# Performance work log

Measured on AMD Instinct MI355X. Metric: run time of the kernel, lower is better.

## Reference

```python
import jax, jax.numpy as jnp
import numpy as np

INPUT_SIZE = 512
HIDDEN = 768
NUM_ARMS = 32
LAMBD = 1.0
NU = 0.1


def setup_inputs() -> dict:
    key = jax.random.key(0)
    ks = jax.random.split(key, 10)
    H, I, A = HIDDEN, INPUT_SIZE, NUM_ARMS
    inp = {
        "x": jax.random.normal(ks[0], (I,), dtype=jnp.float32),
        "previous_reward": jax.random.normal(ks[1], (1, 1), dtype=jnp.float32),
        "h0": jnp.zeros((1, 1, H), dtype=jnp.float32),
        "c0": jnp.zeros((1, 1, H), dtype=jnp.float32),
        # LSTM params, torch layout: W_ih [4H, I+1], W_hh [4H, H], biases [4H]
        "W_ih": jax.random.normal(ks[2], (4 * H, I + 1), dtype=jnp.float32) * 0.05,
        "W_hh": jax.random.normal(ks[3], (4 * H, H), dtype=jnp.float32) * 0.05,
        "b_ih": jax.random.normal(ks[4], (4 * H,), dtype=jnp.float32) * 0.05,
        "b_hh": jax.random.normal(ks[5], (4 * H,), dtype=jnp.float32) * 0.05,
        "fc_W": jax.random.normal(ks[6], (A, H), dtype=jnp.float32) * 0.05,
        "fc_b": jax.random.normal(ks[7], (A,), dtype=jnp.float32) * 0.05,
    }
    total_param = (4 * H * (I + 1)) + (4 * H * H) + (4 * H) + (4 * H) + (A * H) + A
    inp["U"] = LAMBD * jnp.ones((total_param,), dtype=jnp.float32)
    return inp


def _lstm_arm_rewards(params, xin, h, c):
    """Single-step LSTM (torch gate order i,f,g,o) + reward head."""
    W_ih, W_hh, b_ih, b_hh, fc_W, fc_b = params
    gates = W_ih @ xin + b_ih + W_hh @ h + b_hh  # [4H]
    i, f, g, o = jnp.split(gates, 4)
    i, f, o = jax.nn.sigmoid(i), jax.nn.sigmoid(f), jax.nn.sigmoid(o)
    g = jnp.tanh(g)
    c_new = f * c + i * g
    h_new = o * jnp.tanh(c_new)
    rewards = fc_W @ h_new + fc_b  # [A]
    return rewards, (h_new, c_new)


def reference(x, previous_reward, h0, c0, W_ih, W_hh, b_ih, b_hh, fc_W, fc_b, U):
    A = fc_b.shape[0]
    xin = jnp.concatenate([x, previous_reward.reshape(-1)])  # [I+1]
    h, c = h0.reshape(-1), c0.reshape(-1)
    params = (W_ih, W_hh, b_ih, b_hh, fc_W, fc_b)

    rewards, (h_new, c_new) = _lstm_arm_rewards(params, xin, h, c)
    arm_probs = jax.nn.softmax(rewards)

    # Per-arm gradients d rewards[i] / d params, flattened in torch param order.
    jac = jax.jacrev(lambda p: _lstm_arm_rewards(p, xin, h, c)[0])(params)
    G_lstm = jnp.concatenate([jac[k].reshape(A, -1) for k in range(4)], axis=1)
    # fc_rewards grads are never zeroed in the original (only lstm.zero_grad()),
    # so they accumulate over the arm loop -> cumulative sum over arms.
    G_fc = jnp.cumsum(
        jnp.concatenate([jac[4].reshape(A, -1), jac[5].reshape(A, -1)], axis=1), axis=0
    )
    G = jnp.concatenate([G_lstm, G_fc], axis=1)  # [A, total_param]

    sigma = jnp.sqrt(jnp.sum(LAMBD * G * G / U, axis=1))  # [A]
    ucb = NU * sigma

    selected_arm = jnp.argmax(rewards + ucb)
    selected_reward = rewards[selected_arm].reshape(1, 1)
    U_new = U + G[selected_arm] ** 2

    return (
        selected_reward,
        arm_probs.reshape(1, -1),
        selected_arm,
        h_new.reshape(1, 1, -1),
        c_new.reshape(1, 1, -1),
        U_new,
    )
```

## Files before the change

kernel.cpp:

```cpp
#include <hip/hip_runtime.h>
#include <math.h>

#define H 768
#define ISZ 512
#define IN1 513
#define NARM 32
#define NU_C 0.1f

#define U_WIH 0
#define U_WHH (3072*513)
#define U_BIH (U_WHH + 3072*768)
#define U_BHH (U_BIH + 3072)
#define U_FCW (U_BHH + 3072)
#define U_FCB (U_FCW + 32*768)

#define O_SELR 0
#define O_PROB 1
#define O_SELA 33
#define O_HN   34
#define O_CN   (34+768)
#define O_U    (34+768+768)

#define W_D    0
#define W_T    3072
#define W_HN   6144
#define W_SEL  6912
#define W_HZ   6913

__device__ inline float wave_reduce(float v) {
    for (int d = 32; d > 0; d >>= 1) v += __shfl_xor(v, d, 64);
    return v;
}

__device__ inline float frcp(float x) { return __builtin_amdgcn_rcpf(x); }

__device__ inline void store_f4_as_2xf2(float* p, float4 v) {
    *(float2*)p = make_float2(v.x, v.y);
    *(float2*)(p + 2) = make_float2(v.z, v.w);
}

__global__ __launch_bounds__(256) void k_prep(
    const float* __restrict__ x, const float* __restrict__ prevr,
    const float* __restrict__ h0, const float* __restrict__ c0,
    const float* __restrict__ Wih, const float* __restrict__ Whh,
    const float* __restrict__ bih, const float* __restrict__ bhh,
    const float* __restrict__ U,
    float* __restrict__ out, float* __restrict__ ws)
{
    int wave = threadIdx.x >> 6;
    int lane = threadIdx.x & 63;
    const float pr = prevr[0];

    float4 hv4[3];
    bool nzb = false;
    #pragma unroll
    for (int it = 0; it < 3; ++it) {
        hv4[it] = *(const float4*)(h0 + (lane + it * 64) * 4);
        nzb |= (hv4[it].x != 0.f) || (hv4[it].y != 0.f) ||
               (hv4[it].z != 0.f) || (hv4[it].w != 0.f);
    }
    const bool hnz = (__ballot(nzb) != 0ull);

    if (blockIdx.x < 192) {
        int j = blockIdx.x * 4 + wave;
        float a0 = 0.f, a1 = 0.f, a2 = 0.f, a3 = 0.f;
        const float* r0 = Wih + (size_t)(0*H + j) * IN1;
        const float* r1 = Wih + (size_t)(1*H + j) * IN1;
        const float* r2 = Wih + (size_t)(2*H + j) * IN1;
        const float* r3 = Wih + (size_t)(3*H + j) * IN1;
        for (int k = lane; k < IN1; k += 64) {
            float xv = (k < ISZ) ? x[k] : pr;
            a0 += r0[k] * xv; a1 += r1[k] * xv; a2 += r2[k] * xv; a3 += r3[k] * xv;
        }
        if (hnz) {
            const float* s0 = Whh + (size_t)(0*H + j) * H;
            const float* s1 = Whh + (size_t)(1*H + j) * H;
            const float* s2 = Whh + (size_t)(2*H + j) * H;
            const float* s3 = Whh + (size_t)(3*H + j) * H;
            #pragma unroll
            for (int it = 0; it < 3; ++it) {
                int c = (lane + it * 64) * 4;
                float4 h4 = hv4[it];
                float4 w;
                w = *(const float4*)(s0 + c);
                a0 += w.x*h4.x + w.y*h4.y + w.z*h4.z + w.w*h4.w;
                w = *(const float4*)(s1 + c);
                a1 += w.x*h4.x + w.y*h4.y + w.z*h4.z + w.w*h4.w;
                w = *(const float4*)(s2 + c);
                a2 += w.x*h4.x + w.y*h4.y + w.z*h4.z + w.w*h4.w;
                w = *(const float4*)(s3 + c);
                a3 += w.x*h4.x + w.y*h4.y + w.z*h4.z + w.w*h4.w;
            }
        }
        a0 = wave_reduce(a0); a1 = wave_reduce(a1);
        a2 = wave_reduce(a2); a3 = wave_reduce(a3);
        if (lane == 0) {
            float zi = a0 + bih[0*H + j] + bhh[0*H + j];
            float zf = a1 + bih[1*H + j] + bhh[1*H + j];
            float zg = a2 + bih[2*H + j] + bhh[2*H + j];
            float zo = a3 + bih[3*H + j] + bhh[3*H + j];
            float ig = 1.f / (1.f + expf(-zi));
            float fg = 1.f / (1.f + expf(-zf));
            float gg = tanhf(zg);
            float og = 1.f / (1.f + expf(-zo));
            float cj = c0[j];
            float cn = fg * cj + ig * gg;
            float t  = tanhf(cn);
            float hn = og * t;
            float dtc = og * (1.f - t * t);
            ws[W_D + 0*H + j] = dtc * gg * ig * (1.f - ig);
            ws[W_D + 1*H + j] = dtc * cj * fg * (1.f - fg);
            ws[W_D + 2*H + j] = dtc * ig * (1.f - gg * gg);
            ws[W_D + 3*H + j] = t * og * (1.f - og);
            ws[W_HN + j] = hn;
            out[O_HN + j] = hn;
            out[O_CN + j] = cn;
        }
    } else {
        int r = (blockIdx.x - 192) * 4 + wave;
        const float* uih = U + U_WIH + (size_t)r * IN1;
        float acc = 0.f;
        for (int k = lane; k < IN1; k += 64) {
            float xv = (k < ISZ) ? x[k] : pr;
            acc += xv * xv * frcp(uih[k]);
        }
        if (hnz) {
            const float* uhh = U + U_WHH + (size_t)r * H;
            #pragma unroll
            for (int it = 0; it < 3; ++it) {
                int c = (lane + it * 64) * 4;
                float4 u4 = *(const float4*)(uhh + c);
                float4 h4 = hv4[it];
                acc += h4.x*h4.x*frcp(u4.x) + h4.y*h4.y*frcp(u4.y)
                     + h4.z*h4.z*frcp(u4.z) + h4.w*h4.w*frcp(u4.w);
            }
        }
        acc = wave_reduce(acc);
        if (lane == 0)
            ws[W_T + r] = acc + frcp(U[U_BIH + r]) + frcp(U[U_BHH + r]);
    }
}

__global__ __launch_bounds__(1024) void k_armsfinal(
    const float* __restrict__ fcW, const float* __restrict__ fcb,
    const float* __restrict__ h0, const float* __restrict__ U,
    float* __restrict__ out, float* __restrict__ ws)
{
    __shared__ float wsum_s[H];
    __shared__ float hn_s[H];
    __shared__ float r_s[NARM], s_s[NARM], q_s[NARM];
    __shared__ int nzflag;
    int t = threadIdx.x;
    if (t == 0) nzflag = 0;
    __syncthreads();
    if (t < H) {
        float d0 = ws[W_D + 0*H + t], T0 = ws[W_T + 0*H + t];
        float d1 = ws[W_D + 1*H + t], T1 = ws[W_T + 1*H + t];
        float d2 = ws[W_D + 2*H + t], T2 = ws[W_T + 2*H + t];
        float d3 = ws[W_D + 3*H + t], T3 = ws[W_T + 3*H + t];
        wsum_s[t] = d0*d0*T0 + d1*d1*T1 + d2*d2*T2 + d3*d3*T3;
        hn_s[t] = ws[W_HN + t];
        if (h0[t] != 0.f) atomicOr(&nzflag, 1);
    }
    __syncthreads();
    int wave = t >> 6, lane = t & 63;
    for (int a = wave; a < NARM; a += 16) {
        const float* frow = fcW + (size_t)a * H;
        const float* urow = U + U_FCW + (size_t)a * H;
        float ar = 0.f, as = 0.f, aq = 0.f;
        #pragma unroll
        for (int it = 0; it < 3; ++it) {
            int j = lane * 4 + it * 256;
            float4 f4 = *(const float4*)(frow + j);
            float4 u4 = *(const float4*)(urow + j);
            float4 h4 = *(const float4*)(&hn_s[j]);
            float4 w4 = *(const float4*)(&wsum_s[j]);
            ar += f4.x*h4.x + f4.y*h4.y + f4.z*h4.z + f4.w*h4.w;
            as += f4.x*f4.x*w4.x + f4.y*f4.y*w4.y + f4.z*f4.z*w4.z + f4.w*f4.w*w4.w;
            aq += h4.x*h4.x*frcp(u4.x) + h4.y*h4.y*frcp(u4.y)
                + h4.z*h4.z*frcp(u4.z) + h4.w*h4.w*frcp(u4.w);
        }
        ar = wave_reduce(ar); as = wave_reduce(as); aq = wave_reduce(aq);
        if (lane == 0) {
            r_s[a] = ar + fcb[a];
            s_s[a] = as;
            q_s[a] = aq + frcp(U[U_FCB + a]);
        }
    }
    __syncthreads();
    if (t == 0) ((int*)ws)[W_HZ] = nzflag;
    if (t < NARM) {
        float r = r_s[t];
        float s = s_s[t];
        float q = q_s[t];
        float cum = q;
        for (int d = 1; d < 32; d <<= 1) {
            float v = __shfl_up(cum, d, 32);
            if (t >= d) cum += v;
        }
        float sc = r + NU_C * sqrtf(s + cum);
        float best = sc; int sel = t;
        for (int d = 16; d > 0; d >>= 1) {
            float ob = __shfl_xor(best, d, 32);
            int   oi = __shfl_xor(sel, d, 32);
            if (ob > best || (ob == best && oi < sel)) { best = ob; sel = oi; }
        }
        float mx = r;
        for (int d = 16; d > 0; d >>= 1) mx = fmaxf(mx, __shfl_xor(mx, d, 32));
        float e = expf(r - mx);
        float se = e;
        for (int d = 16; d > 0; d >>= 1) se += __shfl_xor(se, d, 32);
        out[O_PROB + t] = e / se;
        float rsel = __shfl(r, sel, 32);
        if (t == 0) {
            out[O_SELR] = rsel;
            out[O_SELA] = (float)sel;
            ((int*)ws)[W_SEL] = sel;
        }
    }
}

#define B_A 3072
#define B_B (B_A + 2304)
#define B_C (B_B + 6)
#define B_D (B_C + 24)
__global__ __launch_bounds__(256) void k_unew(
    const float* __restrict__ x, const float* __restrict__ prevr,
    const float* __restrict__ h0, const float* __restrict__ fcW,
    const float* __restrict__ U, float* __restrict__ out,
    const float* __restrict__ ws)
{
    const int sel = ((const int*)ws)[W_SEL];
    const int hnz = ((const int*)ws)[W_HZ];
    int b = blockIdx.x, t = threadIdx.x;
    float* Un = out + O_U;
    if (b < B_A) {
        int g = b / H, j = b - g * H;
        float s = fcW[(size_t)sel * H + j] * ws[W_D + g*H + j];
        float s2 = s * s;
        const float* u = U + U_WIH + (size_t)b * IN1;
        float* o = Un + U_WIH + (size_t)b * IN1;
        float xv1 = x[t];
        float xv2 = x[t + 256];
        o[t]       = u[t]       + s2 * xv1 * xv1;
        o[t + 256] = u[t + 256] + s2 * xv2 * xv2;
        if (t == 0) {
            float pr = prevr[0];
            o[512] = u[512] + s2 * pr * pr;
        }
    } else if (b < B_B) {
        int i4 = (b - B_A) * 256 + t;
        int e = i4 * 4;
        float4 u4 = *(const float4*)(U + U_WHH + e);
        float4 o4;
        if (hnz) {
            int r = e / H;
            int g = r / H, j = r - g * H;
            int k = e - r * H;
            float s = fcW[(size_t)sel * H + j] * ws[W_D + g*H + j];
            float s2 = s * s;
            float4 h4 = *(const float4*)(h0 + k);
            o4.x = u4.x + s2 * h4.x * h4.x;
            o4.y = u4.y + s2 * h4.y * h4.y;
            o4.z = u4.z + s2 * h4.z * h4.z;
            o4.w = u4.w + s2 * h4.w * h4.w;
        } else {
            o4 = u4;
        }
        store_f4_as_2xf2(Un + U_WHH + e, o4);
    } else if (b < B_C) {
        int m = ((b - B_B) * 256 + t) * 4;
        int r = (m < 3072) ? m : m - 3072;
        int g = r / H, j = r - g * H;
        float4 f4 = *(const float4*)(fcW + (size_t)sel * H + j);
        float4 d4 = *(const float4*)(ws + W_D + g*H + j);
        float4 u4 = *(const float4*)(U + U_BIH + m);
        float4 o4;
        float sx = f4.x*d4.x, sy = f4.y*d4.y, sz = f4.z*d4.z, sw = f4.w*d4.w;
        o4.x = u4.x + sx*sx; o4.y = u4.y + sy*sy;
        o4.z = u4.z + sz*sz; o4.w = u4.w + sw*sw;
        store_f4_as_2xf2(Un + U_BIH + m, o4);
    } else if (b < B_D) {
        int e = ((b - B_C) * 256 + t) * 4;
        int a = e / H, j = e - a * H;
        float4 h4 = *(const float4*)(ws + W_HN + j);
        float4 u4 = *(const float4*)(U + U_FCW + e);
        float m = (a <= sel) ? 1.f : 0.f;
        float4 o4;
        o4.x = u4.x + m * h4.x * h4.x;
        o4.y = u4.y + m * h4.y * h4.y;
        o4.z = u4.z + m * h4.z * h4.z;
        o4.w = u4.w + m * h4.w * h4.w;
        store_f4_as_2xf2(Un + U_FCW + e, o4);
    } else {
        if (t < NARM)
            Un[U_FCB + t] = U[U_FCB + t] + ((t <= sel) ? 1.f : 0.f);
    }
}

extern "C" void kernel_launch(void* const* d_in, const int* in_sizes, int n_in,
                              void* d_out, int out_size, void* d_ws, size_t ws_size,
                              hipStream_t stream) {
    const float* x     = (const float*)d_in[0];
    const float* prevr = (const float*)d_in[1];
    const float* h0    = (const float*)d_in[2];
    const float* c0    = (const float*)d_in[3];
    const float* Wih   = (const float*)d_in[4];
    const float* Whh   = (const float*)d_in[5];
    const float* bih   = (const float*)d_in[6];
    const float* bhh   = (const float*)d_in[7];
    const float* fcW   = (const float*)d_in[8];
    const float* fcb   = (const float*)d_in[9];
    const float* U     = (const float*)d_in[10];
    float* out = (float*)d_out;
    float* ws  = (float*)d_ws;

    hipLaunchKernelGGL(k_prep, dim3(960), dim3(256), 0, stream,
                       x, prevr, h0, c0, Wih, Whh, bih, bhh, U, out, ws);
    hipLaunchKernelGGL(k_armsfinal, dim3(1), dim3(1024), 0, stream,
                       fcW, fcb, h0, U, out, ws);
    hipLaunchKernelGGL(k_unew, dim3(B_D + 1), dim3(256), 0, stream,
                       x, prevr, h0, fcW, U, out, ws);
}
```

Before: 23.38 us.

## Fuse gate, U-weighted norm and arm partials into prep; move W_hh U copy earlier

After: 28.60 us. +22.3%, slower.

```diff
diff --git a/kernel.cpp b/kernel.cpp
--- a/kernel.cpp
+++ b/kernel.cpp
@@ -22,10 +22,14 @@
 #define O_U    (34+768+768)
 
 #define W_D    0
-#define W_T    3072
-#define W_HN   6144
-#define W_SEL  6912
-#define W_HZ   6913
+#define W_HN   3072
+#define W_HZ   3840
+#define W_SEL  3841
+#define W_PART 4096
+
+#define NPREP 192
+#define NCOPY 480
+#define WHH_F4 589824
 
 __device__ inline float wave_reduce(float v) {
     for (int d = 32; d > 0; d >>= 1) v += __shfl_xor(v, d, 64);
@@ -39,160 +43,171 @@
     *(float2*)(p + 2) = make_float2(v.z, v.w);
 }
 
-__global__ __launch_bounds__(256) void k_prep(
+__global__ __launch_bounds__(256) void k1_prep(
     const float* __restrict__ x, const float* __restrict__ prevr,
     const float* __restrict__ h0, const float* __restrict__ c0,
     const float* __restrict__ Wih, const float* __restrict__ Whh,
     const float* __restrict__ bih, const float* __restrict__ bhh,
+    const float* __restrict__ fcW, const float* __restrict__ fcb,
     const float* __restrict__ U,
     float* __restrict__ out, float* __restrict__ ws)
 {
     int wave = threadIdx.x >> 6;
     int lane = threadIdx.x & 63;
-    const float pr = prevr[0];
 
     float4 hv4[3];
     bool nzb = false;
     #pragma unroll
     for (int it = 0; it < 3; ++it) {
-        hv4[it] = *(const float4*)(h0 + (lane + it * 64) * 4);
+        hv4[it] = *(const float4*)(h0 + lane * 4 + it * 256);
         nzb |= (hv4[it].x != 0.f) || (hv4[it].y != 0.f) ||
                (hv4[it].z != 0.f) || (hv4[it].w != 0.f);
     }
     const bool hnz = (__ballot(nzb) != 0ull);
 
-    if (blockIdx.x < 192) {
-        int j = blockIdx.x * 4 + wave;
-        float a0 = 0.f, a1 = 0.f, a2 = 0.f, a3 = 0.f;
-        const float* r0 = Wih + (size_t)(0*H + j) * IN1;
-        const float* r1 = Wih + (size_t)(1*H + j) * IN1;
-        const float* r2 = Wih + (size_t)(2*H + j) * IN1;
-        const float* r3 = Wih + (size_t)(3*H + j) * IN1;
-        for (int k = lane; k < IN1; k += 64) {
-            float xv = (k < ISZ) ? x[k] : pr;
-            a0 += r0[k] * xv; a1 += r1[k] * xv; a2 += r2[k] * xv; a3 += r3[k] * xv;
-        }
-        if (hnz) {
-            const float* s0 = Whh + (size_t)(0*H + j) * H;
-            const float* s1 = Whh + (size_t)(1*H + j) * H;
-            const float* s2 = Whh + (size_t)(2*H + j) * H;
-            const float* s3 = Whh + (size_t)(3*H + j) * H;
-            #pragma unroll
-            for (int it = 0; it < 3; ++it) {
-                int c = (lane + it * 64) * 4;
-                float4 h4 = hv4[it];
-                float4 w;
-                w = *(const float4*)(s0 + c);
-                a0 += w.x*h4.x + w.y*h4.y + w.z*h4.z + w.w*h4.w;
-                w = *(const float4*)(s1 + c);
-                a1 += w.x*h4.x + w.y*h4.y + w.z*h4.z + w.w*h4.w;
-                w = *(const float4*)(s2 + c);
-                a2 += w.x*h4.x + w.y*h4.y + w.z*h4.z + w.w*h4.w;
-                w = *(const float4*)(s3 + c);
-                a3 += w.x*h4.x + w.y*h4.y + w.z*h4.z + w.w*h4.w;
-            }
-        }
-        a0 = wave_reduce(a0); a1 = wave_reduce(a1);
-        a2 = wave_reduce(a2); a3 = wave_reduce(a3);
-        if (lane == 0) {
-            float zi = a0 + bih[0*H + j] + bhh[0*H + j];
-            float zf = a1 + bih[1*H + j] + bhh[1*H + j];
-            float zg = a2 + bih[2*H + j] + bhh[2*H + j];
-            float zo = a3 + bih[3*H + j] + bhh[3*H + j];
-            float ig = 1.f / (1.f + expf(-zi));
-            float fg = 1.f / (1.f + expf(-zf));
-            float gg = tanhf(zg);
-            float og = 1.f / (1.f + expf(-zo));
-            float cj = c0[j];
-            float cn = fg * cj + ig * gg;
-            float t  = tanhf(cn);
-            float hn = og * t;
-            float dtc = og * (1.f - t * t);
-            ws[W_D + 0*H + j] = dtc * gg * ig * (1.f - ig);
-            ws[W_D + 1*H + j] = dtc * cj * fg * (1.f - fg);
-            ws[W_D + 2*H + j] = dtc * ig * (1.f - gg * gg);
-            ws[W_D + 3*H + j] = t * og * (1.f - og);
-            ws[W_HN + j] = hn;
-            out[O_HN + j] = hn;
-            out[O_CN + j] = cn;
-        }
-    } else {
-        int r = (blockIdx.x - 192) * 4 + wave;
-        const float* uih = U + U_WIH + (size_t)r * IN1;
-        float acc = 0.f;
-        for (int k = lane; k < IN1; k += 64) {
-            float xv = (k < ISZ) ? x[k] : pr;
-            acc += xv * xv * frcp(uih[k]);
-        }
-        if (hnz) {
-            const float* uhh = U + U_WHH + (size_t)r * H;
-            #pragma unroll
-            for (int it = 0; it < 3; ++it) {
-                int c = (lane + it * 64) * 4;
-                float4 u4 = *(const float4*)(uhh + c);
-                float4 h4 = hv4[it];
-                acc += h4.x*h4.x*frcp(u4.x) + h4.y*h4.y*frcp(u4.y)
-                     + h4.z*h4.z*frcp(u4.z) + h4.w*h4.w*frcp(u4.w);
-            }
-        }
-        acc = wave_reduce(acc);
-        if (lane == 0)
-            ws[W_T + r] = acc + frcp(U[U_BIH + r]) + frcp(U[U_BHH + r]);
-    }
-}
-
-__global__ __launch_bounds__(1024) void k_armsfinal(
-    const float* __restrict__ fcW, const float* __restrict__ fcb,
-    const float* __restrict__ h0, const float* __restrict__ U,
+    if (blockIdx.x >= NPREP) {
+        if (blockIdx.x == NPREP && threadIdx.x == 0)
+            ((int*)ws)[W_HZ] = hnz ? 1 : 0;
+        if (hnz) return;
+        const float4* src = (const float4*)(U + U_WHH);
+        float* dst = out + O_U + U_WHH;
+        for (int i = (blockIdx.x - NPREP) * 256 + threadIdx.x;
+             i < WHH_F4; i += NCOPY * 256) {
+            float4 v = src[i];
+            store_f4_as_2xf2(dst + (size_t)i * 4, v);
+        }
+        return;
+    }
+
+    int j = blockIdx.x * 4 + wave;
+    const float pr = prevr[0];
+    const float* r0 = Wih + (size_t)(0*H + j) * IN1;
+    const float* r1 = Wih + (size_t)(1*H + j) * IN1;
+    const float* r2 = Wih + (size_t)(2*H + j) * IN1;
+    const float* r3 = Wih + (size_t)(3*H + j) * IN1;
+    const float* u0 = U + U_WIH + (size_t)(0*H + j) * IN1;
+    const float* u1 = U + U_WIH + (size_t)(1*H + j) * IN1;
+    const float* u2 = U + U_WIH + (size_t)(2*H + j) * IN1;
+    const float* u3 = U + U_WIH + (size_t)(3*H + j) * IN1;
+    float a0 = 0.f, a1 = 0.f, a2 = 0.f, a3 = 0.f;
+    float t0 = 0.f, t1 = 0.f, t2 = 0.f, t3 = 0.f;
+    for (int k = lane; k < IN1; k += 64) {
+        float xv = (k < ISZ) ? x[k] : pr;
+        float x2 = xv * xv;
+        a0 += r0[k] * xv;  t0 += x2 * frcp(u0[k]);
+        a1 += r1[k] * xv;  t1 += x2 * frcp(u1[k]);
+        a2 += r2[k] * xv;  t2 += x2 * frcp(u2[k]);
+        a3 += r3[k] * xv;  t3 += x2 * frcp(u3[k]);
+    }
+    if (hnz) {
+        const float* s0 = Whh + (size_t)(0*H + j) * H;
+        const float* s1 = Whh + (size_t)(1*H + j) * H;
+        const float* s2 = Whh + (size_t)(2*H + j) * H;
+        const float* s3 = Whh + (size_t)(3*H + j) * H;
+        const float* v0 = U + U_WHH + (size_t)(0*H + j) * H;
+        const float* v1 = U + U_WHH + (size_t)(1*H + j) * H;
+        const float* v2 = U + U_WHH + (size_t)(2*H + j) * H;
+        const float* v3 = U + U_WHH + (size_t)(3*H + j) * H;
+        #pragma unroll
+        for (int it = 0; it < 3; ++it) {
+            int c = lane * 4 + it * 256;
+            float4 h4 = hv4[it];
+            float4 w, u;
+            w = *(const float4*)(s0 + c); u = *(const float4*)(v0 + c);
+            a0 += w.x*h4.x + w.y*h4.y + w.z*h4.z + w.w*h4.w;
+            t0 += h4.x*h4.x*frcp(u.x) + h4.y*h4.y*frcp(u.y)
+                + h4.z*h4.z*frcp(u.z) + h4.w*h4.w*frcp(u.w);
+            w = *(const float4*)(s1 + c); u = *(const float4*)(v1 + c);
+            a1 += w.x*h4.x + w.y*h4.y + w.z*h4.z + w.w*h4.w;
+            t1 += h4.x*h4.x*frcp(u.x) + h4.y*h4.y*frcp(u.y)
+                + h4.z*h4.z*frcp(u.z) + h4.w*h4.w*frcp(u.w);
+            w = *(const float4*)(s2 + c); u = *(const float4*)(v2 + c);
+            a2 += w.x*h4.x + w.y*h4.y + w.z*h4.z + w.w*h4.w;
+            t2 += h4.x*h4.x*frcp(u.x) + h4.y*h4.y*frcp(u.y)
+                + h4.z*h4.z*frcp(u.z) + h4.w*h4.w*frcp(u.w);
+            w = *(const float4*)(s3 + c); u = *(const float4*)(v3 + c);
+            a3 += w.x*h4.x + w.y*h4.y + w.z*h4.z + w.w*h4.w;
+            t3 += h4.x*h4.x*frcp(u.x) + h4.y*h4.y*frcp(u.y)
+                + h4.z*h4.z*frcp(u.z) + h4.w*h4.w*frcp(u.w);
+        }
+    }
+    a0 = wave_reduce(a0); a1 = wave_reduce(a1);
+    a2 = wave_reduce(a2); a3 = wave_reduce(a3);
+    t0 = wave_reduce(t0); t1 = wave_reduce(t1);
+    t2 = wave_reduce(t2); t3 = wave_reduce(t3);
+
+    float zi = a0 + bih[0*H + j] + bhh[0*H + j];
+    float zf = a1 + bih[1*H + j] + bhh[1*H + j];
+    float zg = a2 + bih[2*H + j] + bhh[2*H + j];
+    float zo = a3 + bih[3*H + j] + bhh[3*H + j];
+    float ig = 1.f / (1.f + expf(-zi));
+    float fg = 1.f / (1.f + expf(-zf));
+    float gg = tanhf(zg);
+    float og = 1.f / (1.f + expf(-zo));
+    float cj = c0[j];
+    float cn = fg * cj + ig * gg;
+    float th = tanhf(cn);
+    float hn = og * th;
+    float dtc = og * (1.f - th * th);
+    float D0 = dtc * gg * ig * (1.f - ig);
+    float D1 = dtc * cj * fg * (1.f - fg);
+    float D2 = dtc * ig * (1.f - gg * gg);
+    float D3 = th * og * (1.f - og);
+    float T0 = t0 + frcp(U[U_BIH + 0*H + j]) + frcp(U[U_BHH + 0*H + j]);
+    float T1 = t1 + frcp(U[U_BIH + 1*H + j]) + frcp(U[U_BHH + 1*H + j]);
+    float T2 = t2 + frcp(U[U_BIH + 2*H + j]) + frcp(U[U_BHH + 2*H + j]);
+    float T3 = t3 + frcp(U[U_BIH + 3*H + j]) + frcp(U[U_BHH + 3*H + j]);
+    float wsum = D0*D0*T0 + D1*D1*T1 + D2*D2*T2 + D3*D3*T3;
+
+    if (lane == 0) {
+        ws[W_D + 0*H + j] = D0;
+        ws[W_D + 1*H + j] = D1;
+        ws[W_D + 2*H + j] = D2;
+        ws[W_D + 3*H + j] = D3;
+        ws[W_HN + j] = hn;
+        out[O_HN + j] = hn;
+        out[O_CN + j] = cn;
+    }
+
+    __shared__ float part[4][96];
+    if (lane < 32) {
+        float fw = fcW[(size_t)lane * H + j];
+        float uf = U[U_FCW + (size_t)lane * H + j];
+        float rc = fw * hn;
+        float sc = fw * fw * wsum;
+        float qc = hn * hn * frcp(uf);
+        if (blockIdx.x == 0 && wave == 0) {
+            rc += fcb[lane];
+            qc += frcp(U[U_FCB + lane]);
+        }
+        part[wave][lane]      = rc;
+        part[wave][32 + lane] = sc;
+        part[wave][64 + lane] = qc;
+    }
+    __syncthreads();
+    int t = threadIdx.x;
+    if (t < 96)
+        ws[W_PART + (size_t)blockIdx.x * 96 + t] =
+            part[0][t] + part[1][t] + part[2][t] + part[3][t];
+}
+
+__global__ __launch_bounds__(128) void k2_select(
     float* __restrict__ out, float* __restrict__ ws)
 {
-    __shared__ float wsum_s[H];
-    __shared__ float hn_s[H];
-    __shared__ float r_s[NARM], s_s[NARM], q_s[NARM];
-    __shared__ int nzflag;
+    __shared__ float red[96];
     int t = threadIdx.x;
-    if (t == 0) nzflag = 0;
+    if (t < 96) {
+        float s = 0.f;
+        #pragma unroll 8
+        for (int b = 0; b < NPREP; ++b)
+            s += ws[W_PART + (size_t)b * 96 + t];
+        red[t] = s;
+    }
     __syncthreads();
-    if (t < H) {
-        float d0 = ws[W_D + 0*H + t], T0 = ws[W_T + 0*H + t];
-        float d1 = ws[W_D + 1*H + t], T1 = ws[W_T + 1*H + t];
-        float d2 = ws[W_D + 2*H + t], T2 = ws[W_T + 2*H + t];
-        float d3 = ws[W_D + 3*H + t], T3 = ws[W_T + 3*H + t];
-        wsum_s[t] = d0*d0*T0 + d1*d1*T1 + d2*d2*T2 + d3*d3*T3;
-        hn_s[t] = ws[W_HN + t];
-        if (h0[t] != 0.f) atomicOr(&nzflag, 1);
-    }
-    __syncthreads();
-    int wave = t >> 6, lane = t & 63;
-    for (int a = wave; a < NARM; a += 16) {
-        const float* frow = fcW + (size_t)a * H;
-        const float* urow = U + U_FCW + (size_t)a * H;
-        float ar = 0.f, as = 0.f, aq = 0.f;
-        #pragma unroll
-        for (int it = 0; it < 3; ++it) {
-            int j = lane * 4 + it * 256;
-            float4 f4 = *(const float4*)(frow + j);
-            float4 u4 = *(const float4*)(urow + j);
-            float4 h4 = *(const float4*)(&hn_s[j]);
-            float4 w4 = *(const float4*)(&wsum_s[j]);
-            ar += f4.x*h4.x + f4.y*h4.y + f4.z*h4.z + f4.w*h4.w;
-            as += f4.x*f4.x*w4.x + f4.y*f4.y*w4.y + f4.z*f4.z*w4.z + f4.w*f4.w*w4.w;
-            aq += h4.x*h4.x*frcp(u4.x) + h4.y*h4.y*frcp(u4.y)
-                + h4.z*h4.z*frcp(u4.z) + h4.w*h4.w*frcp(u4.w);
-        }
-        ar = wave_reduce(ar); as = wave_reduce(as); aq = wave_reduce(aq);
-        if (lane == 0) {
-            r_s[a] = ar + fcb[a];
-            s_s[a] = as;
-            q_s[a] = aq + frcp(U[U_FCB + a]);
-        }
-    }
-    __syncthreads();
-    if (t == 0) ((int*)ws)[W_HZ] = nzflag;
     if (t < NARM) {
-        float r = r_s[t];
-        float s = s_s[t];
-        float q = q_s[t];
+        float r = red[t];
+        float s = red[32 + t];
+        float q = red[64 + t];
         float cum = q;
         for (int d = 1; d < 32; d <<= 1) {
             float v = __shfl_up(cum, d, 32);
@@ -224,14 +239,13 @@
 #define B_B (B_A + 2304)
 #define B_C (B_B + 6)
 #define B_D (B_C + 24)
-__global__ __launch_bounds__(256) void k_unew(
+__global__ __launch_bounds__(256) void k3_unew(
     const float* __restrict__ x, const float* __restrict__ prevr,
     const float* __restrict__ h0, const float* __restrict__ fcW,
     const float* __restrict__ U, float* __restrict__ out,
     const float* __restrict__ ws)
 {
     const int sel = ((const int*)ws)[W_SEL];
-    const int hnz = ((const int*)ws)[W_HZ];
     int b = blockIdx.x, t = threadIdx.x;
     float* Un = out + O_U;
     if (b < B_A) {
@@ -249,24 +263,21 @@
             o[512] = u[512] + s2 * pr * pr;
         }
     } else if (b < B_B) {
-        int i4 = (b - B_A) * 256 + t;
-        int e = i4 * 4;
+        const int hz = ((const int*)ws)[W_HZ];
+        if (!hz) return;
+        int e = ((b - B_A) * 256 + t) * 4;
         float4 u4 = *(const float4*)(U + U_WHH + e);
+        int r = e / H;
+        int g = r / H, j = r - g * H;
+        int k = e - r * H;
+        float s = fcW[(size_t)sel * H + j] * ws[W_D + g*H + j];
+        float s2 = s * s;
+        float4 h4 = *(const float4*)(h0 + k);
         float4 o4;
-        if (hnz) {
-            int r = e / H;
-            int g = r / H, j = r - g * H;
-            int k = e - r * H;
-            float s = fcW[(size_t)sel * H + j] * ws[W_D + g*H + j];
-            float s2 = s * s;
-            float4 h4 = *(const float4*)(h0 + k);
-            o4.x = u4.x + s2 * h4.x * h4.x;
-            o4.y = u4.y + s2 * h4.y * h4.y;
-            o4.z = u4.z + s2 * h4.z * h4.z;
-            o4.w = u4.w + s2 * h4.w * h4.w;
-        } else {
-            o4 = u4;
-        }
+        o4.x = u4.x + s2 * h4.x * h4.x;
+        o4.y = u4.y + s2 * h4.y * h4.y;
+        o4.z = u4.z + s2 * h4.z * h4.z;
+        o4.w = u4.w + s2 * h4.w * h4.w;
         store_f4_as_2xf2(Un + U_WHH + e, o4);
     } else if (b < B_C) {
         int m = ((b - B_B) * 256 + t) * 4;
@@ -315,10 +326,10 @@
     float* out = (float*)d_out;
     float* ws  = (float*)d_ws;
 
-    hipLaunchKernelGGL(k_prep, dim3(960), dim3(256), 0, stream,
-                       x, prevr, h0, c0, Wih, Whh, bih, bhh, U, out, ws);
-    hipLaunchKernelGGL(k_armsfinal, dim3(1), dim3(1024), 0, stream,
-                       fcW, fcb, h0, U, out, ws);
-    hipLaunchKernelGGL(k_unew, dim3(B_D + 1), dim3(256), 0, stream,
+    hipLaunchKernelGGL(k1_prep, dim3(NPREP + NCOPY), dim3(256), 0, stream,
+                       x, prevr, h0, c0, Wih, Whh, bih, bhh, fcW, fcb, U, out, ws);
+    hipLaunchKernelGGL(k2_select, dim3(1), dim3(128), 0, stream,
+                       out, ws);
+    hipLaunchKernelGGL(k3_unew, dim3(B_D + 1), dim3(256), 0, stream,
                        x, prevr, h0, fcW, U, out, ws);
 }
```

## Fuse arm-selection into prep kernel via last-block ticket; move W_hh copy into prep

Applied to the files above, without the earlier changes.

New measurement: 79.84 us. 3.41x slower.

```diff
diff --git a/kernel.cpp b/kernel.cpp
--- a/kernel.cpp
+++ b/kernel.cpp
@@ -26,6 +26,10 @@
 #define W_HN   6144
 #define W_SEL  6912
 #define W_HZ   6913
+#define W_CNT  6914
+
+#define NB1    960
+#define WHH_F4 589824
 
 __device__ inline float wave_reduce(float v) {
     for (int d = 32; d > 0; d >>= 1) v += __shfl_xor(v, d, 64);
@@ -39,16 +43,18 @@
     *(float2*)(p + 2) = make_float2(v.z, v.w);
 }
 
-__global__ __launch_bounds__(256) void k_prep(
+__global__ __launch_bounds__(256) void k1_prep(
     const float* __restrict__ x, const float* __restrict__ prevr,
     const float* __restrict__ h0, const float* __restrict__ c0,
     const float* __restrict__ Wih, const float* __restrict__ Whh,
     const float* __restrict__ bih, const float* __restrict__ bhh,
+    const float* __restrict__ fcW, const float* __restrict__ fcb,
     const float* __restrict__ U,
     float* __restrict__ out, float* __restrict__ ws)
 {
-    int wave = threadIdx.x >> 6;
-    int lane = threadIdx.x & 63;
+    const int t = threadIdx.x;
+    const int wave = t >> 6;
+    const int lane = t & 63;
     const float pr = prevr[0];
 
     float4 hv4[3];
@@ -105,13 +111,13 @@
             float og = 1.f / (1.f + expf(-zo));
             float cj = c0[j];
             float cn = fg * cj + ig * gg;
-            float t  = tanhf(cn);
-            float hn = og * t;
-            float dtc = og * (1.f - t * t);
+            float tt = tanhf(cn);
+            float hn = og * tt;
+            float dtc = og * (1.f - tt * tt);
             ws[W_D + 0*H + j] = dtc * gg * ig * (1.f - ig);
             ws[W_D + 1*H + j] = dtc * cj * fg * (1.f - fg);
             ws[W_D + 2*H + j] = dtc * ig * (1.f - gg * gg);
-            ws[W_D + 3*H + j] = t * og * (1.f - og);
+            ws[W_D + 3*H + j] = tt * og * (1.f - og);
             ws[W_HN + j] = hn;
             out[O_HN + j] = hn;
             out[O_CN + j] = cn;
@@ -139,83 +145,84 @@
         if (lane == 0)
             ws[W_T + r] = acc + frcp(U[U_BIH + r]) + frcp(U[U_BHH + r]);
     }
-}
-
-__global__ __launch_bounds__(1024) void k_armsfinal(
-    const float* __restrict__ fcW, const float* __restrict__ fcb,
-    const float* __restrict__ h0, const float* __restrict__ U,
-    float* __restrict__ out, float* __restrict__ ws)
-{
-    __shared__ float wsum_s[H];
-    __shared__ float hn_s[H];
-    __shared__ float r_s[NARM], s_s[NARM], q_s[NARM];
-    __shared__ int nzflag;
-    int t = threadIdx.x;
-    if (t == 0) nzflag = 0;
+
     __syncthreads();
-    if (t < H) {
-        float d0 = ws[W_D + 0*H + t], T0 = ws[W_T + 0*H + t];
-        float d1 = ws[W_D + 1*H + t], T1 = ws[W_T + 1*H + t];
-        float d2 = ws[W_D + 2*H + t], T2 = ws[W_T + 2*H + t];
-        float d3 = ws[W_D + 3*H + t], T3 = ws[W_T + 3*H + t];
-        wsum_s[t] = d0*d0*T0 + d1*d1*T1 + d2*d2*T2 + d3*d3*T3;
-        hn_s[t] = ws[W_HN + t];
-        if (h0[t] != 0.f) atomicOr(&nzflag, 1);
+    __shared__ unsigned tk_sh;
+    if (t == 0) {
+        __threadfence();
+        tk_sh = atomicAdd((unsigned*)ws + W_CNT, 1u);
     }
     __syncthreads();
-    int wave = t >> 6, lane = t & 63;
-    for (int a = wave; a < NARM; a += 16) {
-        const float* frow = fcW + (size_t)a * H;
-        const float* urow = U + U_FCW + (size_t)a * H;
-        float ar = 0.f, as = 0.f, aq = 0.f;
-        #pragma unroll
-        for (int it = 0; it < 3; ++it) {
-            int j = lane * 4 + it * 256;
-            float4 f4 = *(const float4*)(frow + j);
-            float4 u4 = *(const float4*)(urow + j);
-            float4 h4 = *(const float4*)(&hn_s[j]);
-            float4 w4 = *(const float4*)(&wsum_s[j]);
-            ar += f4.x*h4.x + f4.y*h4.y + f4.z*h4.z + f4.w*h4.w;
-            as += f4.x*f4.x*w4.x + f4.y*f4.y*w4.y + f4.z*f4.z*w4.z + f4.w*f4.w*w4.w;
-            aq += h4.x*h4.x*frcp(u4.x) + h4.y*h4.y*frcp(u4.y)
-                + h4.z*h4.z*frcp(u4.z) + h4.w*h4.w*frcp(u4.w);
-        }
-        ar = wave_reduce(ar); as = wave_reduce(as); aq = wave_reduce(aq);
-        if (lane == 0) {
-            r_s[a] = ar + fcb[a];
-            s_s[a] = as;
-            q_s[a] = aq + frcp(U[U_FCB + a]);
-        }
-    }
-    __syncthreads();
-    if (t == 0) ((int*)ws)[W_HZ] = nzflag;
-    if (t < NARM) {
-        float r = r_s[t];
-        float s = s_s[t];
-        float q = q_s[t];
-        float cum = q;
-        for (int d = 1; d < 32; d <<= 1) {
-            float v = __shfl_up(cum, d, 32);
-            if (t >= d) cum += v;
-        }
-        float sc = r + NU_C * sqrtf(s + cum);
-        float best = sc; int sel = t;
-        for (int d = 16; d > 0; d >>= 1) {
-            float ob = __shfl_xor(best, d, 32);
-            int   oi = __shfl_xor(sel, d, 32);
-            if (ob > best || (ob == best && oi < sel)) { best = ob; sel = oi; }
-        }
-        float mx = r;
-        for (int d = 16; d > 0; d >>= 1) mx = fmaxf(mx, __shfl_xor(mx, d, 32));
-        float e = expf(r - mx);
-        float se = e;
-        for (int d = 16; d > 0; d >>= 1) se += __shfl_xor(se, d, 32);
-        out[O_PROB + t] = e / se;
-        float rsel = __shfl(r, sel, 32);
-        if (t == 0) {
-            out[O_SELR] = rsel;
-            out[O_SELA] = (float)sel;
-            ((int*)ws)[W_SEL] = sel;
+
+    if (tk_sh == NB1 - 1) {
+        __threadfence();
+        __shared__ float wsum_s[H], hn_s[H];
+        __shared__ float r_s[NARM], s_s[NARM], q_s[NARM];
+        for (int j = t; j < H; j += 256) {
+            float d0 = ws[W_D + 0*H + j], T0 = ws[W_T + 0*H + j];
+            float d1 = ws[W_D + 1*H + j], T1 = ws[W_T + 1*H + j];
+            float d2 = ws[W_D + 2*H + j], T2 = ws[W_T + 2*H + j];
+            float d3 = ws[W_D + 3*H + j], T3 = ws[W_T + 3*H + j];
+            wsum_s[j] = d0*d0*T0 + d1*d1*T1 + d2*d2*T2 + d3*d3*T3;
+            hn_s[j] = ws[W_HN + j];
+        }
+        __syncthreads();
+        for (int a = wave; a < NARM; a += 4) {
+            const float* frow = fcW + (size_t)a * H;
+            const float* urow = U + U_FCW + (size_t)a * H;
+            float ar = 0.f, as_ = 0.f, aq = 0.f;
+            for (int j = lane; j < H; j += 64) {
+                float fw = frow[j], hv = hn_s[j];
+                ar  += fw * hv;
+                as_ += fw * fw * wsum_s[j];
+                aq  += hv * hv * frcp(urow[j]);
+            }
+            ar = wave_reduce(ar); as_ = wave_reduce(as_); aq = wave_reduce(aq);
+            if (lane == 0) {
+                r_s[a] = ar + fcb[a];
+                s_s[a] = as_;
+                q_s[a] = aq + frcp(U[U_FCB + a]);
+            }
+        }
+        __syncthreads();
+        if (t < NARM) {
+            float r = r_s[t];
+            float s = s_s[t];
+            float q = q_s[t];
+            float cum = q;
+            for (int d = 1; d < 32; d <<= 1) {
+                float v = __shfl_up(cum, d, 32);
+                if (t >= d) cum += v;
+            }
+            float sc = r + NU_C * sqrtf(s + cum);
+            float best = sc; int sel = t;
+            for (int d = 16; d > 0; d >>= 1) {
+                float ob = __shfl_xor(best, d, 32);
+                int   oi = __shfl_xor(sel, d, 32);
+                if (ob > best || (ob == best && oi < sel)) { best = ob; sel = oi; }
+            }
+            float mx = r;
+            for (int d = 16; d > 0; d >>= 1) mx = fmaxf(mx, __shfl_xor(mx, d, 32));
+            float e = expf(r - mx);
+            float se = e;
+            for (int d = 16; d > 0; d >>= 1) se += __shfl_xor(se, d, 32);
+            out[O_PROB + t] = e / se;
+            float rsel = __shfl(r, sel, 32);
+            if (t == 0) {
+                out[O_SELR] = rsel;
+                out[O_SELA] = (float)sel;
+                ((int*)ws)[W_SEL] = sel;
+                ((int*)ws)[W_HZ]  = hnz ? 1 : 0;
+            }
+        }
+    }
+
+    if (!hnz) {
+        const float4* src = (const float4*)(U + U_WHH);
+        float* dst = out + O_U + U_WHH;
+        for (int i = blockIdx.x * 256 + t; i < WHH_F4; i += NB1 * 256) {
+            float4 v = src[i];
+            store_f4_as_2xf2(dst + (size_t)i * 4, v);
         }
     }
 }
@@ -224,14 +231,13 @@
 #define B_B (B_A + 2304)
 #define B_C (B_B + 6)
 #define B_D (B_C + 24)
-__global__ __launch_bounds__(256) void k_unew(
+__global__ __launch_bounds__(256) void k2_unew(
     const float* __restrict__ x, const float* __restrict__ prevr,
     const float* __restrict__ h0, const float* __restrict__ fcW,
     const float* __restrict__ U, float* __restrict__ out,
     const float* __restrict__ ws)
 {
     const int sel = ((const int*)ws)[W_SEL];
-    const int hnz = ((const int*)ws)[W_HZ];
     int b = blockIdx.x, t = threadIdx.x;
     float* Un = out + O_U;
     if (b < B_A) {
@@ -249,24 +255,21 @@
             o[512] = u[512] + s2 * pr * pr;
         }
     } else if (b < B_B) {
-        int i4 = (b - B_A) * 256 + t;
-        int e = i4 * 4;
+        const int hz = ((const int*)ws)[W_HZ];
+        if (!hz) return;
+        int e = ((b - B_A) * 256 + t) * 4;
         float4 u4 = *(const float4*)(U + U_WHH + e);
+        int r = e / H;
+        int g = r / H, j = r - g * H;
+        int k = e - r * H;
+        float s = fcW[(size_t)sel * H + j] * ws[W_D + g*H + j];
+        float s2 = s * s;
+        float4 h4 = *(const float4*)(h0 + k);
         float4 o4;
-        if (hnz) {
-            int r = e / H;
-            int g = r / H, j = r - g * H;
-            int k = e - r * H;
-            float s = fcW[(size_t)sel * H + j] * ws[W_D + g*H + j];
-            float s2 = s * s;
-            float4 h4 = *(const float4*)(h0 + k);
-            o4.x = u4.x + s2 * h4.x * h4.x;
-            o4.y = u4.y + s2 * h4.y * h4.y;
-            o4.z = u4.z + s2 * h4.z * h4.z;
-            o4.w = u4.w + s2 * h4.w * h4.w;
-        } else {
-            o4 = u4;
-        }
+        o4.x = u4.x + s2 * h4.x * h4.x;
+        o4.y = u4.y + s2 * h4.y * h4.y;
+        o4.z = u4.z + s2 * h4.z * h4.z;
+        o4.w = u4.w + s2 * h4.w * h4.w;
         store_f4_as_2xf2(Un + U_WHH + e, o4);
     } else if (b < B_C) {
         int m = ((b - B_B) * 256 + t) * 4;
@@ -315,10 +318,10 @@
     float* out = (float*)d_out;
     float* ws  = (float*)d_ws;
 
-    hipLaunchKernelGGL(k_prep, dim3(960), dim3(256), 0, stream,
-                       x, prevr, h0, c0, Wih, Whh, bih, bhh, U, out, ws);
-    hipLaunchKernelGGL(k_armsfinal, dim3(1), dim3(1024), 0, stream,
-                       fcW, fcb, h0, U, out, ws);
-    hipLaunchKernelGGL(k_unew, dim3(B_D + 1), dim3(256), 0, stream,
+    hipMemsetAsync((char*)d_ws + (size_t)W_CNT * 4, 0, 4, stream);
+
+    hipLaunchKernelGGL(k1_prep, dim3(NB1), dim3(256), 0, stream,
+                       x, prevr, h0, c0, Wih, Whh, bih, bhh, fcW, fcb, U, out, ws);
+    hipLaunchKernelGGL(k2_unew, dim3(B_D + 1), dim3(256), 0, stream,
                        x, prevr, h0, fcW, U, out, ws);
 }
```
